# Performance work log

Hardware: AMD Instinct MI355X
Metric: run time of the kernel (lower is better)

Reference implementation:

```python
import jax, jax.numpy as jnp
import numpy as np

_K_MASK = float(jnp.finfo(jnp.float32).min)
EPS = 1e-6
B, T, D = 2, 2048, 2048
NH, NKV, HD = 16, 4, 128


def _rope_tables(key):
    # Standard RoPE tables: (B, T, HD) with [freqs, freqs] layout (rotate_half convention)
    inv_freq = 1.0 / (10000.0 ** (np.arange(0, HD, 2, dtype=np.float32) / HD))  # (HD/2,)
    pos = np.arange(T, dtype=np.float32)
    freqs = np.einsum('t,f->tf', pos, inv_freq)              # (T, HD/2)
    emb = np.concatenate([freqs, freqs], axis=-1)            # (T, HD)
    cos = jnp.broadcast_to(jnp.cos(emb)[None], (B, T, HD))
    sin = jnp.broadcast_to(jnp.sin(emb)[None], (B, T, HD))
    return cos, sin


def setup_inputs() -> dict:
    key = jax.random.key(0)
    ks = jax.random.split(key, 6)
    s = 0.02
    cos, sin = _rope_tables(key)
    return {
        'x': jax.random.normal(ks[0], (B, T, D), jnp.float32),
        'cos': cos,
        'sin': sin,
        'wq': jax.random.normal(ks[1], (D, NH * HD * 2), jnp.float32) * s,
        'wk': jax.random.normal(ks[2], (D, NKV * HD), jnp.float32) * s,
        'wv': jax.random.normal(ks[3], (D, NKV * HD), jnp.float32) * s,
        'wo': jax.random.normal(ks[4], (NH * HD, D), jnp.float32) * s,
        'q_norm_w': jnp.ones((HD,), jnp.float32),
        'k_norm_w': jnp.ones((HD,), jnp.float32),
        'segment_ids': jnp.ones((B, T), jnp.int32),
        'position_ids': jnp.broadcast_to(jnp.arange(T, dtype=jnp.int32)[None], (B, T)),
    }


def _rmsnorm(x, w):
    var = jnp.mean(jnp.square(x.astype(jnp.float32)), axis=-1, keepdims=True)
    return (x.astype(jnp.float32) * jax.lax.rsqrt(var + EPS)).astype(x.dtype) * w


def _rotate_half(x):
    x1, x2 = jnp.split(x, 2, axis=-1)
    return jnp.concatenate([-x2, x1], axis=-1)


def _apply_rope(q, k, cos, sin):
    # q: (B, NH, T, HD), k: (B, NKV, T, HD), cos/sin: (B, T, HD)
    c = cos[:, None, :, :]
    s = sin[:, None, :, :]
    q = q * c + _rotate_half(q) * s
    k = k * c + _rotate_half(k) * s
    return q, k


def reference(x, cos, sin, wq, wk, wv, wo, q_norm_w, k_norm_w, segment_ids, position_ids):
    Bx, Tx, _ = x.shape
    n_rep = NH // NKV
    scale = HD ** -0.5

    q_out = (x @ wq).reshape(Bx, Tx, NH, HD * 2)
    query, gate = jnp.split(q_out, 2, axis=-1)         # each (B, T, NH, HD)
    gate = gate.reshape(Bx, Tx, -1)                    # (B, T, NH*HD)
    query = _rmsnorm(query, q_norm_w).transpose(0, 2, 1, 3)   # (B, NH, T, HD)
    key = _rmsnorm((x @ wk).reshape(Bx, Tx, NKV, HD), k_norm_w).transpose(0, 2, 1, 3)
    value = (x @ wv).reshape(Bx, Tx, NKV, HD).transpose(0, 2, 1, 3)

    query, key = _apply_rope(query, key, cos, sin)
    if n_rep > 1:
        key = jnp.repeat(key, n_rep, axis=1)
        value = jnp.repeat(value, n_rep, axis=1)

    attn_logits = jnp.einsum('bhqd,bhkd->bhqk', query, key) * scale
    causal = position_ids[:, :, None] >= position_ids[:, None, :]
    seg = segment_ids[:, :, None] == segment_ids[:, None, :]
    mask = (causal & seg)[:, None, :, :]
    attn_logits = jnp.where(mask, attn_logits, _K_MASK)
    attn_weights = jax.nn.softmax(attn_logits.astype(jnp.float32), axis=-1).astype(attn_logits.dtype)
    attn_out = jnp.einsum('bhqk,bhkd->bhqd', attn_weights, value)
    attn_out = attn_out.transpose(0, 2, 1, 3).reshape(Bx, Tx, -1)  # (B, T, NH*HD)
    attn_out = attn_out * jax.nn.sigmoid(gate)
    return attn_out @ wo
```

## Files before the change

### kernel.cpp

```cpp
#include <hip/hip_runtime.h>

#define AS1 __attribute__((address_space(1)))
#define AS3 __attribute__((address_space(3)))

typedef __bf16 bf16x8 __attribute__((ext_vector_type(8)));
typedef float f32x4 __attribute__((ext_vector_type(4)));
typedef float f32x16 __attribute__((ext_vector_type(16)));
typedef unsigned short us8 __attribute__((ext_vector_type(8)));
typedef unsigned int u32x4 __attribute__((ext_vector_type(4)));

static constexpr int T_ = 2048;
static constexpr int NH_ = 16;
static constexpr int NKV_ = 4;
static constexpr int HD_ = 128;
static constexpr int NQKV_ = 5120;
static constexpr float SL2E_ = 0.12751744f;

static __device__ __forceinline__ unsigned short f2b(float f) {
  unsigned u = __builtin_bit_cast(unsigned, f);
  u += 0x7fffu + ((u >> 16) & 1u);
  return (unsigned short)(u >> 16);
}
static __device__ __forceinline__ void load_lds16(const void* g, void* l) {
  __builtin_amdgcn_global_load_lds((const AS1 unsigned int*)g, (AS3 unsigned int*)l, 16, 0, 0);
}
static __device__ __forceinline__ f32x4 mfma16(bf16x8 a, bf16x8 b, f32x4 c) {
  return __builtin_amdgcn_mfma_f32_16x16x32_bf16(a, b, c, 0, 0, 0);
}
static __device__ __forceinline__ f32x16 mfma32(bf16x8 a, bf16x8 b, f32x16 c) {
  return __builtin_amdgcn_mfma_f32_32x32x16_bf16(a, b, c, 0, 0, 0);
}
static __device__ __forceinline__ unsigned cvtpk(float lo, float hi) {
  unsigned r;
  asm("v_cvt_pk_bf16_f32 %0, %1, %2" : "=v"(r) : "v"(lo), "v"(hi));
  return r;
}
static __device__ __forceinline__ void pl32swap(unsigned& a, unsigned& b) {
  asm("v_permlane32_swap_b32 %0, %1" : "+v"(a), "+v"(b));
}
#define S_BARRIER() asm volatile("s_barrier" ::: "memory")

__global__ __launch_bounds__(256) void conv_bf16_kernel(
    const float* __restrict__ src, unsigned short* __restrict__ dst, int n) {
  int i = (blockIdx.x * 256 + threadIdx.x) * 4;
  if (i >= n) return;
  float4 v = *(const float4*)(src + i);
  ushort4 o;
  o.x = f2b(v.x); o.y = f2b(v.y); o.z = f2b(v.z); o.w = f2b(v.w);
  *(ushort4*)(dst + i) = o;
}

__global__ void tconv_kernel(const float* __restrict__ src, unsigned short* __restrict__ dst,
                             int R, int C, int roff) {
  __shared__ float tile[32][33];
  const int c0 = blockIdx.x * 32, r0 = blockIdx.y * 32;
#pragma unroll
  for (int j = 0; j < 32; j += 8)
    tile[threadIdx.y + j][threadIdx.x] =
        src[(size_t)(r0 + threadIdx.y + j) * C + c0 + threadIdx.x];
  __syncthreads();
#pragma unroll
  for (int j = 0; j < 32; j += 8)
    dst[(size_t)(roff + c0 + threadIdx.y + j) * R + r0 + threadIdx.x] =
        f2b(tile[threadIdx.x][threadIdx.y + j]);
}

__global__ void vtrans_kernel(const float* __restrict__ qkv, unsigned short* __restrict__ Vt) {
  __shared__ unsigned short tile[32][33];
  const int bh = blockIdx.z;
  const int b = bh >> 2, vh = bh & 3;
  const int d0 = blockIdx.x * 32, t0 = blockIdx.y * 32;
#pragma unroll
  for (int j = 0; j < 32; j += 8) {
    const int t = t0 + threadIdx.y + j;
    tile[threadIdx.y + j][threadIdx.x] =
        f2b(qkv[(size_t)(b * T_ + t) * NQKV_ + 4608 + vh * 128 + d0 + threadIdx.x]);
  }
  __syncthreads();
  unsigned short* dst = Vt + (size_t)bh * HD_ * T_;
#pragma unroll
  for (int j = 0; j < 32; j += 8)
    dst[(size_t)(d0 + threadIdx.y + j) * T_ + t0 + threadIdx.x] =
        tile[threadIdx.x][threadIdx.y + j];
}

__global__ __launch_bounds__(512, 2) void gemm256_kernel(
    const unsigned short* __restrict__ A, const unsigned short* __restrict__ Bt,
    float* __restrict__ C, int K, int N) {
  __shared__ __align__(16) unsigned short As[2][256 * 64];
  __shared__ __align__(16) unsigned short Bs[2][256 * 64];
  const int gw = N >> 8;
  const int nwg = gridDim.x;
  int bid = blockIdx.x;
  bid = (bid & 7) * (nwg >> 3) + (bid >> 3);
  const int brow = (bid / gw) * 256, bcol = (bid % gw) * 256;

  const int tid = threadIdx.x;
  const int wid = tid >> 6, lane = tid & 63;
  const int lq = lane & 15, lg = lane >> 4;
  const int wr = wid >> 2, wc = wid & 3;

  f32x4 acc[8][4];
#pragma unroll
  for (int m = 0; m < 8; ++m)
#pragma unroll
    for (int n = 0; n < 4; ++n) acc[m][n] = (f32x4){0.f, 0.f, 0.f, 0.f};

  auto STAGE2 = [&](const unsigned short* __restrict__ M, int brc, int t,
                    unsigned short* buf, int half) {
    const int k0 = t * 64;
#pragma unroll
    for (int j = 0; j < 2; ++j) {
      const int ch = half * 16 + j * 8 + wid;
      const int row = ch * 8 + (lane >> 3);
      load_lds16(M + (size_t)(brc + row) * K + k0 + (((lane & 7) ^ (row & 7)) << 3),
                 buf + (ch << 9));
    }
  };
  auto RD_A = [&](int p, int m, int ks) -> bf16x8 {
    const int r = wr * 128 + m * 16 + lq;
    return *(const bf16x8*)&As[p][r * 64 + (((ks * 4 + lg) ^ (r & 7)) << 3)];
  };
  auto RD_B = [&](int p, int n, int ks) -> bf16x8 {
    const int r = wc * 64 + n * 16 + lq;
    return *(const bf16x8*)&Bs[p][r * 64 + (((ks * 4 + lg) ^ (r & 7)) << 3)];
  };

  STAGE2(A, brow, 0, &As[0][0], 0);  STAGE2(A, brow, 0, &As[0][0], 1);
  STAGE2(Bt, bcol, 0, &Bs[0][0], 0); STAGE2(Bt, bcol, 0, &Bs[0][0], 1);
  STAGE2(Bt, bcol, 1, &Bs[1][0], 0); STAGE2(Bt, bcol, 1, &Bs[1][0], 1);
  asm volatile("s_waitcnt vmcnt(4)" ::: "memory");
  __builtin_amdgcn_s_barrier();

  const int NT = K >> 6;
  for (int t = 0; t < NT; ++t) {
    const int p = t & 1;
    unsigned short* Ab = &As[p ^ 1][0];
    unsigned short* Bb = &Bs[p][0];
    bf16x8 aL[4][2], aH[4][2], bL[2][2], bH[2][2];
#pragma unroll
    for (int m = 0; m < 4; ++m)
#pragma unroll
      for (int ks = 0; ks < 2; ++ks) aL[m][ks] = RD_A(p, m, ks);
#pragma unroll
    for (int n = 0; n < 2; ++n)
#pragma unroll
      for (int ks = 0; ks < 2; ++ks) bL[n][ks] = RD_B(p, n, ks);
    if (t < NT - 1) STAGE2(A, brow, t + 1, Ab, 0);
    __builtin_amdgcn_s_barrier();
    __builtin_amdgcn_sched_barrier(0);
    __builtin_amdgcn_s_setprio(1);
#pragma unroll
    for (int m = 0; m < 4; ++m)
#pragma unroll
      for (int n = 0; n < 2; ++n) {
        acc[m][n] = mfma16(aL[m][0], bL[n][0], acc[m][n]);
        acc[m][n] = mfma16(aL[m][1], bL[n][1], acc[m][n]);
      }
    __builtin_amdgcn_s_setprio(0);
    __builtin_amdgcn_s_barrier();
#pragma unroll
    for (int n = 0; n < 2; ++n)
#pragma unroll
      for (int ks = 0; ks < 2; ++ks) bH[n][ks] = RD_B(p, n + 2, ks);
    if (t < NT - 1) STAGE2(A, brow, t + 1, Ab, 1);
    __builtin_amdgcn_s_barrier();
    __builtin_amdgcn_sched_barrier(0);
    __builtin_amdgcn_s_setprio(1);
#pragma unroll
    for (int m = 0; m < 4; ++m)
#pragma unroll
      for (int n = 0; n < 2; ++n) {
        acc[m][n + 2] = mfma16(aL[m][0], bH[n][0], acc[m][n + 2]);
        acc[m][n + 2] = mfma16(aL[m][1], bH[n][1], acc[m][n + 2]);
      }
    __builtin_amdgcn_s_setprio(0);
    __builtin_amdgcn_s_barrier();
#pragma unroll
    for (int m = 0; m < 4; ++m)
#pragma unroll
      for (int ks = 0; ks < 2; ++ks) aH[m][ks] = RD_A(p, m + 4, ks);
    if (t < NT - 2) STAGE2(Bt, bcol, t + 2, Bb, 0);
    __builtin_amdgcn_s_barrier();
    __builtin_amdgcn_sched_barrier(0);
    __builtin_amdgcn_s_setprio(1);
#pragma unroll
    for (int m = 0; m < 4; ++m)
#pragma unroll
      for (int n = 0; n < 2; ++n) {
        acc[m + 4][n + 2] = mfma16(aH[m][0], bH[n][0], acc[m + 4][n + 2]);
        acc[m + 4][n + 2] = mfma16(aH[m][1], bH[n][1], acc[m + 4][n + 2]);
      }
    __builtin_amdgcn_s_setprio(0);
    __builtin_amdgcn_s_barrier();
    if (t < NT - 2) {
      STAGE2(Bt, bcol, t + 2, Bb, 1);
      asm volatile("s_waitcnt vmcnt(4)" ::: "memory");
    } else if (t == NT - 2) {
      asm volatile("s_waitcnt vmcnt(0)" ::: "memory");
    }
    __builtin_amdgcn_s_barrier();
    __builtin_amdgcn_sched_barrier(0);
    __builtin_amdgcn_s_setprio(1);
#pragma unroll
    for (int m = 0; m < 4; ++m)
#pragma unroll
      for (int n = 0; n < 2; ++n) {
        acc[m + 4][n] = mfma16(aH[m][0], bL[n][0], acc[m + 4][n]);
        acc[m + 4][n] = mfma16(aH[m][1], bL[n][1], acc[m + 4][n]);
      }
    __builtin_amdgcn_s_setprio(0);
    __builtin_amdgcn_s_barrier();
  }
#pragma unroll
  for (int m = 0; m < 8; ++m)
#pragma unroll
    for (int n = 0; n < 4; ++n)
#pragma unroll
      for (int r = 0; r < 4; ++r)
        C[(size_t)(brow + wr * 128 + m * 16 + lg * 4 + r) * N + bcol + wc * 64 + n * 16 + lq] =
            acc[m][n][r];
}

__global__ __launch_bounds__(512, 2) void gemm_bt8_kernel(
    const unsigned short* __restrict__ A, const unsigned short* __restrict__ Bt,
    float* __restrict__ C, int K, int N) {
  __shared__ __align__(16) unsigned short As[3][128 * 64];
  __shared__ __align__(16) unsigned short Bs[3][256 * 64];
  const int tid = threadIdx.x;
  const int wid = tid >> 6, lane = tid & 63;
  const int lq = lane & 15, lg = lane >> 4;
  const int l8 = lane >> 3, s8 = lane & 7;
  const int wr = wid >> 2, wc = wid & 3;
  const int brow = blockIdx.y * 128, bcol = blockIdx.x * 256;

  f32x4 acc[4][4];
#pragma unroll
  for (int m = 0; m < 4; ++m)
#pragma unroll
    for (int n = 0; n < 4; ++n) acc[m][n] = (f32x4){0.f, 0.f, 0.f, 0.f};

  auto STAGE_HALF = [&](int t, int b3t, int half) {
    const int k0 = t * 64;
    {
      const int ca = wid + half * 8;
      const int row = ca * 8 + l8;
      load_lds16(A + (size_t)(brow + row) * K + k0 + ((s8 ^ (row & 7)) << 3),
                 &As[b3t][ca << 9]);
    }
#pragma unroll
    for (int j = 0; j < 2; ++j) {
      const int cb = wid + half * 16 + (j << 3);
      const int row = cb * 8 + l8;
      load_lds16(Bt + (size_t)(bcol + row) * K + k0 + ((s8 ^ (row & 7)) << 3),
                 &Bs[b3t][cb << 9]);
    }
  };
  auto PHASE_READS = [&](int b3, int ks, bf16x8* a, bf16x8* bb) {
#pragma unroll
    for (int m = 0; m < 4; ++m) {
      const int r = wr * 64 + m * 16 + lq;
      a[m] = *(const bf16x8*)&As[b3][r * 64 + (((ks * 4 + lg) ^ (r & 7)) << 3)];
    }
#pragma unroll
    for (int n = 0; n < 4; ++n) {
      const int r = wc * 64 + n * 16 + lq;
      bb[n] = *(const bf16x8*)&Bs[b3][r * 64 + (((ks * 4 + lg) ^ (r & 7)) << 3)];
    }
  };
  auto DO_MFMA = [&](bf16x8* a, bf16x8* bb) {
    __builtin_amdgcn_s_setprio(1);
#pragma unroll
    for (int m = 0; m < 4; ++m)
#pragma unroll
      for (int n = 0; n < 4; ++n) acc[m][n] = mfma16(a[m], bb[n], acc[m][n]);
    __builtin_amdgcn_s_setprio(0);
  };

  STAGE_HALF(0, 0, 0); STAGE_HALF(0, 0, 1);
  STAGE_HALF(1, 1, 0); STAGE_HALF(1, 1, 1);
  asm volatile("s_waitcnt vmcnt(6)" ::: "memory");
  S_BARRIER();

  int b3 = 0;
  for (int t = 0; t < 32; ++t) {
    const int b3p2 = b3 < 1 ? b3 + 2 : b3 - 1;
    bf16x8 a[4], bb[4];
    PHASE_READS(b3, 0, a, bb);
    if (t < 30) STAGE_HALF(t + 2, b3p2, 0);
    S_BARRIER();
    __builtin_amdgcn_sched_barrier(0);
    DO_MFMA(a, bb);
    S_BARRIER();
    PHASE_READS(b3, 1, a, bb);
    if (t < 30) STAGE_HALF(t + 2, b3p2, 1);
    if (t < 30) {
      asm volatile("s_waitcnt vmcnt(6)" ::: "memory");
    } else if (t == 30) {
      asm volatile("s_waitcnt vmcnt(0)" ::: "memory");
    }
    S_BARRIER();
    __builtin_amdgcn_sched_barrier(0);
    DO_MFMA(a, bb);
    if (t < 31) S_BARRIER();
    b3 = b3 < 2 ? b3 + 1 : 0;
  }
#pragma unroll
  for (int m = 0; m < 4; ++m)
#pragma unroll
    for (int n = 0; n < 4; ++n)
#pragma unroll
      for (int r = 0; r < 4; ++r)
        C[(size_t)(brow + wr * 64 + m * 16 + lg * 4 + r) * N + bcol + wc * 64 + n * 16 + lq] =
            acc[m][n][r];
}

__global__ __launch_bounds__(256) void postproc_kernel(
    const float* __restrict__ qkv, const float* __restrict__ cosT,
    const float* __restrict__ sinT, const float* __restrict__ qnw,
    const float* __restrict__ knw, unsigned short* __restrict__ Qg,
    unsigned short* __restrict__ Kg) {
  const int row = blockIdx.x;
  const int b = row >> 11, t = row & 2047;
  const float* src = qkv + (size_t)row * NQKV_;
  const int tid = threadIdx.x;
  const int sub = tid & 15;
  const int i0 = sub * 8;
  const bool lo = sub < 8;

  float cs[8], sn[8];
#pragma unroll
  for (int j = 0; j < 8; ++j) {
    cs[j] = cosT[(size_t)row * HD_ + i0 + j];
    sn[j] = sinT[(size_t)row * HD_ + i0 + j];
  }
  {
    const int h = tid >> 4;
    float q[8], ss = 0.f;
#pragma unroll
    for (int j = 0; j < 8; ++j) { q[j] = src[h * 256 + i0 + j]; ss += q[j] * q[j]; }
    ss += __shfl_xor(ss, 1); ss += __shfl_xor(ss, 2);
    ss += __shfl_xor(ss, 4); ss += __shfl_xor(ss, 8);
    const float rms = rsqrtf(ss * (1.f / 128.f) + 1e-6f);
    float qn[8];
#pragma unroll
    for (int j = 0; j < 8; ++j) qn[j] = q[j] * rms * qnw[i0 + j];
    float pr[8];
#pragma unroll
    for (int j = 0; j < 8; ++j) pr[j] = __shfl_xor(qn[j], 8);
    us8 ov;
#pragma unroll
    for (int j = 0; j < 8; ++j) ov[j] = f2b(qn[j] * cs[j] + (lo ? -pr[j] : pr[j]) * sn[j]);
    *(us8*)(Qg + ((size_t)(b * NH_ + h) * T_ + t) * HD_ + i0) = ov;
  }
  if (tid < 64) {
    const int kh = tid >> 4;
    float k[8], ss = 0.f;
#pragma unroll
    for (int j = 0; j < 8; ++j) { k[j] = src[4096 + kh * 128 + i0 + j]; ss += k[j] * k[j]; }
    ss += __shfl_xor(ss, 1); ss += __shfl_xor(ss, 2);
    ss += __shfl_xor(ss, 4); ss += __shfl_xor(ss, 8);
    const float rms = rsqrtf(ss * (1.f / 128.f) + 1e-6f);
    float kn[8];
#pragma unroll
    for (int j = 0; j < 8; ++j) kn[j] = k[j] * rms * knw[i0 + j];
    float pr[8];
#pragma unroll
    for (int j = 0; j < 8; ++j) pr[j] = __shfl_xor(kn[j], 8);
    us8 ov;
#pragma unroll
    for (int j = 0; j < 8; ++j) ov[j] = f2b(kn[j] * cs[j] + (lo ? -pr[j] : pr[j]) * sn[j]);
    *(us8*)(Kg + ((size_t)(b * NKV_ + kh) * T_ + t) * HD_ + i0) = ov;
  }
}

__global__ __launch_bounds__(256, 2) void attn_kernel(
    const unsigned short* __restrict__ Qg, const unsigned short* __restrict__ Kg,
    const unsigned short* __restrict__ Vt, const float* __restrict__ qkv,
    unsigned short* __restrict__ attnb) {
  __shared__ __align__(16) char smem[65536];
  const int i = blockIdx.x;
  const int xi = (i >> 3) & 15;
  const int grp = (i & 7) + ((i >> 7) << 3);
  const int h = grp & 15, b = grp >> 4;
  const int qt = b ? (15 - xi) : xi;
  const int kh = h >> 2;
  const int tid = threadIdx.x, wid = tid >> 6, lane = tid & 63;
  const int lq = lane & 31, hi = lane >> 5;
  const int q0 = qt * 128;
  const int qbase = q0 + wid * 32;
  const int qrow = qbase + lq;

  bf16x8 qf[8];
  const unsigned short* qptr = Qg + ((size_t)(b * NH_ + h) * T_ + qrow) * HD_;
#pragma unroll
  for (int t = 0; t < 8; ++t) qf[t] = *(const bf16x8*)(qptr + t * 16 + hi * 8);

  const char* Kbase = (const char*)(Kg + (size_t)(b * NKV_ + kh) * T_ * HD_);
  const char* Vbase = (const char*)(Vt + (size_t)(b * NKV_ + kh) * HD_ * T_);

  f32x16 o[4];
#pragma unroll
  for (int d = 0; d < 4; ++d)
#pragma unroll
    for (int r = 0; r < 16; ++r) o[d][r] = 0.f;
  float m_r = -1e30f, l_r = 0.f;
  const int nt = 2 * qt + 2;

  auto STAGE = [&](int tt, int c) {
    const int t0 = tt * 64;
    char* kd = smem + c * 32768;
    char* vd = kd + 16384;
#pragma unroll
    for (int j = 0; j < 4; ++j) {
      const int ch = j * 4 + wid;
      const int kv = ch * 4 + (lane >> 4);
      load_lds16(Kbase + (size_t)(t0 + kv) * 256 + (((lane & 15) ^ (kv & 7)) << 4),
                 kd + ch * 1024);
      const int dv = ch * 8 + (lane >> 3);
      load_lds16(Vbase + (size_t)dv * (T_ * 2) + (size_t)t0 * 2 +
                     (((lane & 7) ^ (dv & 7)) << 4),
                 vd + ch * 1024);
    }
  };

  STAGE(0, 0);
  __syncthreads();
  int cur = 0;
  for (int tt = 0; tt < nt; ++tt) {
    const int t0 = tt * 64;
    if (tt + 1 < nt) STAGE(tt + 1, cur ^ 1);
    if (t0 <= qbase + 31) {
      const char* kd = smem + cur * 32768;
      const char* vd = kd + 16384;
      f32x16 sA, sB;
#pragma unroll
      for (int r = 0; r < 16; ++r) { sA[r] = 0.f; sB[r] = 0.f; }
      __builtin_amdgcn_s_setprio(1);
#pragma unroll
      for (int t = 0; t < 8; ++t) {
        const int sw = t * 2 + hi;
        bf16x8 ka = *(const bf16x8*)(kd + lq * 256 + ((sw ^ (lq & 7)) << 4));
        bf16x8 kb = *(const bf16x8*)(kd + (lq + 32) * 256 + ((sw ^ (lq & 7)) << 4));
        sA = mfma32(ka, qf[t], sA);
        sB = mfma32(kb, qf[t], sB);
      }
      __builtin_amdgcn_s_setprio(0);
      float p[32];
      float mx = -1e30f;
      const bool anymask = (t0 + 63 > qbase);
#pragma unroll
      for (int r = 0; r < 16; ++r) {
        const int kv = (r & 3) + ((r >> 2) << 3) + hi * 4;
        float vA = sA[r] * SL2E_;
        float vB = sB[r] * SL2E_;
        if (anymask) {
          if (t0 + kv > qrow) vA = -1e30f;
          if (t0 + kv + 32 > qrow) vB = -1e30f;
        }
        p[r] = vA; p[16 + r] = vB;
        mx = fmaxf(mx, fmaxf(vA, vB));
      }
      mx = fmaxf(mx, __shfl_xor(mx, 32));
      const float mn = fmaxf(m_r, mx);
      const float al = exp2f(m_r - mn);
      float sum = 0.f;
#pragma unroll
      for (int j = 0; j < 32; ++j) { p[j] = exp2f(p[j] - mn); sum += p[j]; }
      sum += __shfl_xor(sum, 32);
      l_r = l_r * al + sum;
      m_r = mn;
#pragma unroll
      for (int d = 0; d < 4; ++d)
#pragma unroll
        for (int r = 0; r < 16; ++r) o[d][r] *= al;
      bf16x8 pf[4];
#pragma unroll
      for (int kt = 0; kt < 4; ++kt) {
        const float* pp = p + kt * 8;
        unsigned a0 = cvtpk(pp[0], pp[1]);
        unsigned a1 = cvtpk(pp[2], pp[3]);
        unsigned b0 = cvtpk(pp[4], pp[5]);
        unsigned b1 = cvtpk(pp[6], pp[7]);
        pl32swap(a0, b0);
        pl32swap(a1, b1);
        u32x4 w = {a0, a1, b0, b1};
        pf[kt] = __builtin_bit_cast(bf16x8, w);
      }
      __builtin_amdgcn_s_setprio(1);
#pragma unroll
      for (int dt = 0; dt < 4; ++dt) {
        const int d = dt * 32 + lq;
#pragma unroll
        for (int kt = 0; kt < 4; ++kt) {
          bf16x8 vf = *(const bf16x8*)(vd + d * 128 + (((kt * 2 + hi) ^ (d & 7)) << 4));
          o[dt] = mfma32(vf, pf[kt], o[dt]);
        }
      }
      __builtin_amdgcn_s_setprio(0);
    }
    __syncthreads();
    cur ^= 1;
  }
  const float inv = 1.f / l_r;
  const float* grow = qkv + (size_t)(b * T_ + qrow) * NQKV_ + h * 256 + 128;
  unsigned short* orow = attnb + (size_t)(b * T_ + qrow) * (NH_ * HD_) + h * HD_;
#pragma unroll
  for (int dt = 0; dt < 4; ++dt)
#pragma unroll
    for (int g = 0; g < 4; ++g) {
      const int d0 = dt * 32 + g * 8 + hi * 4;
      float4 gv = *(const float4*)(grow + d0);
      ushort4 ov;
      ov.x = f2b(o[dt][g * 4 + 0] * inv / (1.f + __expf(-gv.x)));
      ov.y = f2b(o[dt][g * 4 + 1] * inv / (1.f + __expf(-gv.y)));
      ov.z = f2b(o[dt][g * 4 + 2] * inv / (1.f + __expf(-gv.z)));
      ov.w = f2b(o[dt][g * 4 + 3] * inv / (1.f + __expf(-gv.w)));
      *(ushort4*)(orow + d0) = ov;
    }
}

extern "C" void kernel_launch(void* const* d_in, const int* in_sizes, int n_in,
                              void* d_out, int out_size, void* d_ws, size_t ws_size,
                              hipStream_t stream) {
  (void)in_sizes; (void)n_in; (void)out_size; (void)ws_size;
  const float* x    = (const float*)d_in[0];
  const float* cosT = (const float*)d_in[1];
  const float* sinT = (const float*)d_in[2];
  const float* wq   = (const float*)d_in[3];
  const float* wk   = (const float*)d_in[4];
  const float* wv   = (const float*)d_in[5];
  const float* wo   = (const float*)d_in[6];
  const float* qnw  = (const float*)d_in[7];
  const float* knw  = (const float*)d_in[8];
  float* out = (float*)d_out;
  char* ws = (char*)d_ws;

  constexpr size_t OFF_XB    = 0;
  constexpr size_t OFF_WQKVT = OFF_XB    + (size_t)4096 * 2048 * 2;
  constexpr size_t OFF_WOT   = OFF_WQKVT + (size_t)5120 * 2048 * 2;
  constexpr size_t OFF_QKV   = OFF_WOT   + (size_t)2048 * 2048 * 2;
  constexpr size_t OFF_QG    = OFF_QKV   + (size_t)4096 * 5120 * 4;
  constexpr size_t OFF_KG    = OFF_QG    + (size_t)2 * 16 * 2048 * 128 * 2;
  constexpr size_t OFF_VT    = OFF_KG    + (size_t)2 * 4 * 2048 * 128 * 2;
  constexpr size_t OFF_ATTNB = OFF_VT    + (size_t)2 * 4 * 128 * 2048 * 2;

  unsigned short* xb    = (unsigned short*)(ws + OFF_XB);
  unsigned short* wqkvT = (unsigned short*)(ws + OFF_WQKVT);
  unsigned short* woT   = (unsigned short*)(ws + OFF_WOT);
  float*          qkv   = (float*)(ws + OFF_QKV);
  unsigned short* Qg    = (unsigned short*)(ws + OFF_QG);
  unsigned short* Kg    = (unsigned short*)(ws + OFF_KG);
  unsigned short* Vt    = (unsigned short*)(ws + OFF_VT);
  unsigned short* attnb = (unsigned short*)(ws + OFF_ATTNB);

  const int nX = 4096 * 2048;
  conv_bf16_kernel<<<nX / 4 / 256, 256, 0, stream>>>(x, xb, nX);
  tconv_kernel<<<dim3(4096 / 32, 2048 / 32), dim3(32, 8), 0, stream>>>(wq, wqkvT, 2048, 4096, 0);
  tconv_kernel<<<dim3(512 / 32, 2048 / 32), dim3(32, 8), 0, stream>>>(wk, wqkvT, 2048, 512, 4096);
  tconv_kernel<<<dim3(512 / 32, 2048 / 32), dim3(32, 8), 0, stream>>>(wv, wqkvT, 2048, 512, 4608);
  tconv_kernel<<<dim3(2048 / 32, 2048 / 32), dim3(32, 8), 0, stream>>>(wo, woT, 2048, 2048, 0);

  gemm256_kernel<<<320, 512, 0, stream>>>(xb, wqkvT, qkv, 2048, 5120);

  postproc_kernel<<<4096, 256, 0, stream>>>(qkv, cosT, sinT, qnw, knw, Qg, Kg);
  vtrans_kernel<<<dim3(128 / 32, 2048 / 32, 8), dim3(32, 8), 0, stream>>>(qkv, Vt);

  attn_kernel<<<512, 256, 0, stream>>>(Qg, Kg, Vt, qkv, attnb);

  gemm_bt8_kernel<<<dim3(2048 / 256, 4096 / 128), 512, 0, stream>>>(attnb, woT, out, 2048, 2048);
}
```

Before: 295.4 us.

## Retile QKV GEMM to 256x320 and rework output GEMM pipeline and XCD mapping

```diff
diff --git a/kernel.cpp b/kernel.cpp
--- a/kernel.cpp
+++ b/kernel.cpp
@@ -38,7 +38,7 @@
 static __device__ __forceinline__ void pl32swap(unsigned& a, unsigned& b) {
   asm("v_permlane32_swap_b32 %0, %1" : "+v"(a), "+v"(b));
 }
-#define S_BARRIER() asm volatile("s_barrier" ::: "memory")
+#define VMCNT(n) asm volatile("s_waitcnt vmcnt(" #n ")" ::: "memory")
 
 __global__ __launch_bounds__(256) void conv_bf16_kernel(
     const float* __restrict__ src, unsigned short* __restrict__ dst, int n) {
@@ -84,69 +84,64 @@
         tile[threadIdx.x][threadIdx.y + j];
 }
 
-__global__ __launch_bounds__(512, 2) void gemm256_kernel(
+__global__ __launch_bounds__(512, 2) void gemm1_kernel(
     const unsigned short* __restrict__ A, const unsigned short* __restrict__ Bt,
     float* __restrict__ C, int K, int N) {
   __shared__ __align__(16) unsigned short As[2][256 * 64];
-  __shared__ __align__(16) unsigned short Bs[2][256 * 64];
-  const int gw = N >> 8;
-  const int nwg = gridDim.x;
-  int bid = blockIdx.x;
-  bid = (bid & 7) * (nwg >> 3) + (bid >> 3);
-  const int brow = (bid / gw) * 256, bcol = (bid % gw) * 256;
-
-  const int tid = threadIdx.x;
-  const int wid = tid >> 6, lane = tid & 63;
+  __shared__ __align__(16) unsigned short Bs[2][320 * 64];
+  const int bid = blockIdx.x;
+  const int xcd = bid & 7, c = bid >> 3;
+  const int brow = (((xcd & 1) << 3) + (c & 7)) * 256;
+  const int bcol = (((xcd >> 1) << 2) + (c >> 3)) * 320;
+  const int tid = threadIdx.x, wid = tid >> 6, lane = tid & 63;
   const int lq = lane & 15, lg = lane >> 4;
   const int wr = wid >> 2, wc = wid & 3;
-
-  f32x4 acc[8][4];
+  const int srow = lane >> 3, spc = lane & 7;
+  const int ssw = (spc ^ srow) << 3;
+  const int sw0 = ((lg) ^ (lq & 7)) << 3;
+  const int sw1 = ((4 + lg) ^ (lq & 7)) << 3;
+
+  f32x4 acc[8][5];
 #pragma unroll
   for (int m = 0; m < 8; ++m)
 #pragma unroll
-    for (int n = 0; n < 4; ++n) acc[m][n] = (f32x4){0.f, 0.f, 0.f, 0.f};
-
-  auto STAGE2 = [&](const unsigned short* __restrict__ M, int brc, int t,
-                    unsigned short* buf, int half) {
-    const int k0 = t * 64;
-#pragma unroll
-    for (int j = 0; j < 2; ++j) {
-      const int ch = half * 16 + j * 8 + wid;
-      const int row = ch * 8 + (lane >> 3);
-      load_lds16(M + (size_t)(brc + row) * K + k0 + (((lane & 7) ^ (row & 7)) << 3),
-                 buf + (ch << 9));
+    for (int n = 0; n < 5; ++n) acc[m][n] = (f32x4){0.f, 0.f, 0.f, 0.f};
+
+  auto STAGE_A = [&](int t) {
+    const int k0 = t << 6, p = t & 1;
+#pragma unroll
+    for (int j = 0; j < 4; ++j) {
+      const int ch = wid * 4 + j;
+      load_lds16(A + (size_t)(brow + ch * 8 + srow) * K + k0 + ssw, &As[p][ch << 9]);
+    }
+  };
+  auto STAGE_B = [&](int t, int j0, int j1) {
+    const int k0 = t << 6, p = t & 1;
+    for (int j = j0; j < j1; ++j) {
+      const int ch = wid * 5 + j;
+      load_lds16(Bt + (size_t)(bcol + ch * 8 + srow) * K + k0 + ssw, &Bs[p][ch << 9]);
     }
   };
   auto RD_A = [&](int p, int m, int ks) -> bf16x8 {
-    const int r = wr * 128 + m * 16 + lq;
-    return *(const bf16x8*)&As[p][r * 64 + (((ks * 4 + lg) ^ (r & 7)) << 3)];
+    return *(const bf16x8*)&As[p][(wr * 128 + m * 16 + lq) * 64 + (ks ? sw1 : sw0)];
   };
   auto RD_B = [&](int p, int n, int ks) -> bf16x8 {
-    const int r = wc * 64 + n * 16 + lq;
-    return *(const bf16x8*)&Bs[p][r * 64 + (((ks * 4 + lg) ^ (r & 7)) << 3)];
-  };
-
-  STAGE2(A, brow, 0, &As[0][0], 0);  STAGE2(A, brow, 0, &As[0][0], 1);
-  STAGE2(Bt, bcol, 0, &Bs[0][0], 0); STAGE2(Bt, bcol, 0, &Bs[0][0], 1);
-  STAGE2(Bt, bcol, 1, &Bs[1][0], 0); STAGE2(Bt, bcol, 1, &Bs[1][0], 1);
-  asm volatile("s_waitcnt vmcnt(4)" ::: "memory");
+    return *(const bf16x8*)&Bs[p][(wc * 80 + n * 16 + lq) * 64 + (ks ? sw1 : sw0)];
+  };
+
+  STAGE_A(0); STAGE_B(0, 0, 5); STAGE_B(1, 0, 5);
+  VMCNT(5);
   __builtin_amdgcn_s_barrier();
 
   const int NT = K >> 6;
   for (int t = 0; t < NT; ++t) {
     const int p = t & 1;
-    unsigned short* Ab = &As[p ^ 1][0];
-    unsigned short* Bb = &Bs[p][0];
-    bf16x8 aL[4][2], aH[4][2], bL[2][2], bH[2][2];
-#pragma unroll
-    for (int m = 0; m < 4; ++m)
-#pragma unroll
-      for (int ks = 0; ks < 2; ++ks) aL[m][ks] = RD_A(p, m, ks);
-#pragma unroll
-    for (int n = 0; n < 2; ++n)
-#pragma unroll
-      for (int ks = 0; ks < 2; ++ks) bL[n][ks] = RD_B(p, n, ks);
-    if (t < NT - 1) STAGE2(A, brow, t + 1, Ab, 0);
+    bf16x8 aL[4][2], aH[4][2], bL[2][2], bH[3][2];
+#pragma unroll
+    for (int m = 0; m < 4; ++m) { aL[m][0] = RD_A(p, m, 0); aL[m][1] = RD_A(p, m, 1); }
+#pragma unroll
+    for (int n = 0; n < 2; ++n) { bL[n][0] = RD_B(p, n, 0); bL[n][1] = RD_B(p, n, 1); }
+    if (t < NT - 1) STAGE_A(t + 1);
     __builtin_amdgcn_s_barrier();
     __builtin_amdgcn_sched_barrier(0);
     __builtin_amdgcn_s_setprio(1);
@@ -160,44 +155,39 @@
     __builtin_amdgcn_s_setprio(0);
     __builtin_amdgcn_s_barrier();
 #pragma unroll
-    for (int n = 0; n < 2; ++n)
-#pragma unroll
-      for (int ks = 0; ks < 2; ++ks) bH[n][ks] = RD_B(p, n + 2, ks);
-    if (t < NT - 1) STAGE2(A, brow, t + 1, Ab, 1);
+    for (int n = 0; n < 3; ++n) { bH[n][0] = RD_B(p, n + 2, 0); bH[n][1] = RD_B(p, n + 2, 1); }
     __builtin_amdgcn_s_barrier();
     __builtin_amdgcn_sched_barrier(0);
     __builtin_amdgcn_s_setprio(1);
 #pragma unroll
     for (int m = 0; m < 4; ++m)
 #pragma unroll
-      for (int n = 0; n < 2; ++n) {
+      for (int n = 0; n < 3; ++n) {
         acc[m][n + 2] = mfma16(aL[m][0], bH[n][0], acc[m][n + 2]);
         acc[m][n + 2] = mfma16(aL[m][1], bH[n][1], acc[m][n + 2]);
       }
     __builtin_amdgcn_s_setprio(0);
     __builtin_amdgcn_s_barrier();
 #pragma unroll
-    for (int m = 0; m < 4; ++m)
-#pragma unroll
-      for (int ks = 0; ks < 2; ++ks) aH[m][ks] = RD_A(p, m + 4, ks);
-    if (t < NT - 2) STAGE2(Bt, bcol, t + 2, Bb, 0);
+    for (int m = 0; m < 4; ++m) { aH[m][0] = RD_A(p, m + 4, 0); aH[m][1] = RD_A(p, m + 4, 1); }
+    if (t < NT - 2) STAGE_B(t + 2, 0, 3);
     __builtin_amdgcn_s_barrier();
     __builtin_amdgcn_sched_barrier(0);
     __builtin_amdgcn_s_setprio(1);
 #pragma unroll
     for (int m = 0; m < 4; ++m)
 #pragma unroll
-      for (int n = 0; n < 2; ++n) {
+      for (int n = 0; n < 3; ++n) {
         acc[m + 4][n + 2] = mfma16(aH[m][0], bH[n][0], acc[m + 4][n + 2]);
         acc[m + 4][n + 2] = mfma16(aH[m][1], bH[n][1], acc[m + 4][n + 2]);
       }
     __builtin_amdgcn_s_setprio(0);
     __builtin_amdgcn_s_barrier();
     if (t < NT - 2) {
-      STAGE2(Bt, bcol, t + 2, Bb, 1);
-      asm volatile("s_waitcnt vmcnt(4)" ::: "memory");
-    } else if (t == NT - 2) {
-      asm volatile("s_waitcnt vmcnt(0)" ::: "memory");
+      STAGE_B(t + 2, 3, 5);
+      VMCNT(5);
+    } else {
+      VMCNT(0);
     }
     __builtin_amdgcn_s_barrier();
     __builtin_amdgcn_sched_barrier(0);
@@ -215,24 +205,29 @@
 #pragma unroll
   for (int m = 0; m < 8; ++m)
 #pragma unroll
-    for (int n = 0; n < 4; ++n)
+    for (int n = 0; n < 5; ++n)
 #pragma unroll
       for (int r = 0; r < 4; ++r)
-        C[(size_t)(brow + wr * 128 + m * 16 + lg * 4 + r) * N + bcol + wc * 64 + n * 16 + lq] =
+        C[(size_t)(brow + wr * 128 + m * 16 + lg * 4 + r) * N + bcol + wc * 80 + n * 16 + lq] =
             acc[m][n][r];
 }
 
-__global__ __launch_bounds__(512, 2) void gemm_bt8_kernel(
+__global__ __launch_bounds__(512, 2) void gemm2_kernel(
     const unsigned short* __restrict__ A, const unsigned short* __restrict__ Bt,
     float* __restrict__ C, int K, int N) {
-  __shared__ __align__(16) unsigned short As[3][128 * 64];
-  __shared__ __align__(16) unsigned short Bs[3][256 * 64];
-  const int tid = threadIdx.x;
-  const int wid = tid >> 6, lane = tid & 63;
+  __shared__ __align__(16) unsigned short As[2][128 * 64];
+  __shared__ __align__(16) unsigned short Bs[2][256 * 64];
+  const int bid = blockIdx.x;
+  const int xcd = bid & 7, c = bid >> 3;
+  const int brow = (((xcd & 3) << 3) + (c & 7)) * 128;
+  const int bcol = (((xcd >> 2) << 2) + (c >> 3)) * 256;
+  const int tid = threadIdx.x, wid = tid >> 6, lane = tid & 63;
   const int lq = lane & 15, lg = lane >> 4;
-  const int l8 = lane >> 3, s8 = lane & 7;
   const int wr = wid >> 2, wc = wid & 3;
-  const int brow = blockIdx.y * 128, bcol = blockIdx.x * 256;
+  const int srow = lane >> 3, spc = lane & 7;
+  const int ssw = (spc ^ srow) << 3;
+  const int sw0 = ((lg) ^ (lq & 7)) << 3;
+  const int sw1 = ((4 + lg) ^ (lq & 7)) << 3;
 
   f32x4 acc[4][4];
 #pragma unroll
@@ -240,70 +235,74 @@
 #pragma unroll
     for (int n = 0; n < 4; ++n) acc[m][n] = (f32x4){0.f, 0.f, 0.f, 0.f};
 
-  auto STAGE_HALF = [&](int t, int b3t, int half) {
-    const int k0 = t * 64;
-    {
-      const int ca = wid + half * 8;
-      const int row = ca * 8 + l8;
-      load_lds16(A + (size_t)(brow + row) * K + k0 + ((s8 ^ (row & 7)) << 3),
-                 &As[b3t][ca << 9]);
-    }
+  auto STAGE_A = [&](int t) {
+    const int k0 = t << 6, p = t & 1;
 #pragma unroll
     for (int j = 0; j < 2; ++j) {
-      const int cb = wid + half * 16 + (j << 3);
-      const int row = cb * 8 + l8;
-      load_lds16(Bt + (size_t)(bcol + row) * K + k0 + ((s8 ^ (row & 7)) << 3),
-                 &Bs[b3t][cb << 9]);
-    }
-  };
-  auto PHASE_READS = [&](int b3, int ks, bf16x8* a, bf16x8* bb) {
-#pragma unroll
-    for (int m = 0; m < 4; ++m) {
-      const int r = wr * 64 + m * 16 + lq;
-      a[m] = *(const bf16x8*)&As[b3][r * 64 + (((ks * 4 + lg) ^ (r & 7)) << 3)];
-    }
-#pragma unroll
-    for (int n = 0; n < 4; ++n) {
-      const int r = wc * 64 + n * 16 + lq;
-      bb[n] = *(const bf16x8*)&Bs[b3][r * 64 + (((ks * 4 + lg) ^ (r & 7)) << 3)];
-    }
-  };
-  auto DO_MFMA = [&](bf16x8* a, bf16x8* bb) {
+      const int ch = wid * 2 + j;
+      load_lds16(A + (size_t)(brow + ch * 8 + srow) * K + k0 + ssw, &As[p][ch << 9]);
+    }
+  };
+  auto STAGE_B = [&](int t) {
+    const int k0 = t << 6, p = t & 1;
+#pragma unroll
+    for (int j = 0; j < 4; ++j) {
+      const int ch = wid * 4 + j;
+      load_lds16(Bt + (size_t)(bcol + ch * 8 + srow) * K + k0 + ssw, &Bs[p][ch << 9]);
+    }
+  };
+  auto RD_A = [&](int p, int m, int ks) -> bf16x8 {
+    return *(const bf16x8*)&As[p][(wr * 64 + m * 16 + lq) * 64 + (ks ? sw1 : sw0)];
+  };
+  auto RD_B = [&](int p, int n, int ks) -> bf16x8 {
+    return *(const bf16x8*)&Bs[p][(wc * 64 + n * 16 + lq) * 64 + (ks ? sw1 : sw0)];
+  };
+
+  STAGE_A(0); STAGE_B(0); STAGE_B(1);
+  VMCNT(4);
+  __builtin_amdgcn_s_barrier();
+
+  const int NT = K >> 6;
+  for (int t = 0; t < NT; ++t) {
+    const int p = t & 1;
+    bf16x8 a[4][2], bL[2][2], bH[2][2];
+#pragma unroll
+    for (int m = 0; m < 4; ++m) { a[m][0] = RD_A(p, m, 0); a[m][1] = RD_A(p, m, 1); }
+#pragma unroll
+    for (int n = 0; n < 2; ++n) { bL[n][0] = RD_B(p, n, 0); bL[n][1] = RD_B(p, n, 1); }
+    if (t < NT - 1) STAGE_A(t + 1);
+    __builtin_amdgcn_s_barrier();
+    __builtin_amdgcn_sched_barrier(0);
     __builtin_amdgcn_s_setprio(1);
 #pragma unroll
     for (int m = 0; m < 4; ++m)
 #pragma unroll
-      for (int n = 0; n < 4; ++n) acc[m][n] = mfma16(a[m], bb[n], acc[m][n]);
+      for (int n = 0; n < 2; ++n) {
+        acc[m][n] = mfma16(a[m][0], bL[n][0], acc[m][n]);
+        acc[m][n] = mfma16(a[m][1], bL[n][1], acc[m][n]);
+      }
     __builtin_amdgcn_s_setprio(0);
-  };
-
-  STAGE_HALF(0, 0, 0); STAGE_HALF(0, 0, 1);
-  STAGE_HALF(1, 1, 0); STAGE_HALF(1, 1, 1);
-  asm volatile("s_waitcnt vmcnt(6)" ::: "memory");
-  S_BARRIER();
-
-  int b3 = 0;
-  for (int t = 0; t < 32; ++t) {
-    const int b3p2 = b3 < 1 ? b3 + 2 : b3 - 1;
-    bf16x8 a[4], bb[4];
-    PHASE_READS(b3, 0, a, bb);
-    if (t < 30) STAGE_HALF(t + 2, b3p2, 0);
-    S_BARRIER();
+    __builtin_amdgcn_s_barrier();
+#pragma unroll
+    for (int n = 0; n < 2; ++n) { bH[n][0] = RD_B(p, n + 2, 0); bH[n][1] = RD_B(p, n + 2, 1); }
+    if (t < NT - 2) {
+      STAGE_B(t + 2);
+      VMCNT(4);
+    } else {
+      VMCNT(0);
+    }
+    __builtin_amdgcn_s_barrier();
     __builtin_amdgcn_sched_barrier(0);
-    DO_MFMA(a, bb);
-    S_BARRIER();
-    PHASE_READS(b3, 1, a, bb);
-    if (t < 30) STAGE_HALF(t + 2, b3p2, 1);
-    if (t < 30) {
-      asm volatile("s_waitcnt vmcnt(6)" ::: "memory");
-    } else if (t == 30) {
-      asm volatile("s_waitcnt vmcnt(0)" ::: "memory");
-    }
-    S_BARRIER();
-    __builtin_amdgcn_sched_barrier(0);
-    DO_MFMA(a, bb);
-    if (t < 31) S_BARRIER();
-    b3 = b3 < 2 ? b3 + 1 : 0;
+    __builtin_amdgcn_s_setprio(1);
+#pragma unroll
+    for (int m = 0; m < 4; ++m)
+#pragma unroll
+      for (int n = 0; n < 2; ++n) {
+        acc[m][n + 2] = mfma16(a[m][0], bH[n][0], acc[m][n + 2]);
+        acc[m][n + 2] = mfma16(a[m][1], bH[n][1], acc[m][n + 2]);
+      }
+    __builtin_amdgcn_s_setprio(0);
+    __builtin_amdgcn_s_barrier();
   }
 #pragma unroll
   for (int m = 0; m < 4; ++m)
@@ -561,12 +560,12 @@
   tconv_kernel<<<dim3(512 / 32, 2048 / 32), dim3(32, 8), 0, stream>>>(wv, wqkvT, 2048, 512, 4608);
   tconv_kernel<<<dim3(2048 / 32, 2048 / 32), dim3(32, 8), 0, stream>>>(wo, woT, 2048, 2048, 0);
 
-  gemm256_kernel<<<320, 512, 0, stream>>>(xb, wqkvT, qkv, 2048, 5120);
+  gemm1_kernel<<<256, 512, 0, stream>>>(xb, wqkvT, qkv, 2048, 5120);
 
   postproc_kernel<<<4096, 256, 0, stream>>>(qkv, cosT, sinT, qnw, knw, Qg, Kg);
   vtrans_kernel<<<dim3(128 / 32, 2048 / 32, 8), dim3(32, 8), 0, stream>>>(qkv, Vt);
 
   attn_kernel<<<512, 256, 0, stream>>>(Qg, Kg, Vt, qkv, attnb);
 
-  gemm_bt8_kernel<<<dim3(2048 / 256, 4096 / 128), 512, 0, stream>>>(attnb, woT, out, 2048, 2048);
-}
+  gemm2_kernel<<<256, 512, 0, stream>>>(attnb, woT, out, 2048, 2048);
+}
```

After: 315.6 us. 1.07x slower.
